# Optimization experiments

Hardware: AMD Instinct MI355X
Metric: run time of the kernel (lower is better)

The kernel has to match this reference:

```python
import jax, jax.numpy as jnp
import numpy as np
from jax import lax

K = 3
EPS = 1e-5


def get_graph_feature(x, k):
    # Faithful to the torch code, including flat .view() reshapes (no transpose)
    B, N = x.shape[0], x.shape[1]          # num_points = x.size(1)
    x = x.reshape(B, -1, N)                # (B, C, N) flat reshape
    C = x.shape[1]
    inner = -2.0 * jnp.einsum('bcn,bcm->bnm', x, x)           # (B, N, N)
    xx = jnp.sum(x * x, axis=1, keepdims=True)                # (B, 1, N)
    dist = -xx - inner - jnp.swapaxes(xx, 1, 2)               # neg sq distances
    idx = lax.top_k(dist, k)[1]                               # (B, N, k) nearest
    flat = x.reshape(B * N, C)                                # flat reshape (as torch .view)
    idx_full = (idx + (jnp.arange(B) * N)[:, None, None]).reshape(-1)
    feature = flat[idx_full].reshape(B, N, k, C)
    xc = x.reshape(B, N, 1, C)                                # flat reshape (as torch .view)
    feature = jnp.concatenate([feature - xc, jnp.broadcast_to(xc, (B, N, k, C))], axis=3)
    return feature.reshape(B, 2 * C, k, N)                    # flat reshape (as torch .view)


def bn(h, g, b, m, v, axis):
    shape = [1] * h.ndim
    shape[axis] = -1
    inv = g.reshape(shape) / jnp.sqrt(v.reshape(shape) + EPS)
    return (h - m.reshape(shape)) * inv + b.reshape(shape)


def setup_inputs() -> dict:
    key = jax.random.key(0)
    ks = jax.random.split(key, 24)
    B, N = 8, 4096

    def bn_params(i, c):
        return {
            f'bn{i}_g': jax.random.uniform(ks[4 * (ord(i) % 4)], (c,), jnp.float32) + 0.5,
            f'bn{i}_b': jax.random.normal(jax.random.fold_in(key, 10 + ord(i)), (c,), jnp.float32) * 0.1,
            f'bn{i}_m': jax.random.normal(jax.random.fold_in(key, 20 + ord(i)), (c,), jnp.float32) * 0.1,
            f'bn{i}_v': jax.random.uniform(jax.random.fold_in(key, 30 + ord(i)), (c,), jnp.float32) + 0.5,
        }

    inp = {
        'x': jax.random.normal(ks[0], (B, N, 3), jnp.float32),
        'w1': jax.random.normal(ks[1], (64, 6), jnp.float32) * (1.0 / np.sqrt(6.0)),
        'wA': jax.random.normal(ks[2], (256, 82), jnp.float32) * (1.0 / np.sqrt(82.0)),
        'bA': jax.random.normal(ks[3], (256,), jnp.float32) * 0.01,
        'wB': jax.random.normal(ks[4], (128, 256), jnp.float32) * (1.0 / np.sqrt(256.0)),
        'bB': jax.random.normal(ks[5], (128,), jnp.float32) * 0.01,
        'wC': jax.random.normal(ks[6], (3, 128), jnp.float32) * (1.0 / np.sqrt(128.0)),
        'bC': jax.random.normal(ks[7], (3,), jnp.float32) * 0.01,
    }
    inp.update(bn_params('1', 64))
    inp.update(bn_params('A', 256))
    inp.update(bn_params('B', 128))
    return inp


def reference(x, w1, wA, bA, wB, bB, wC, bC,
              bn1_g, bn1_b, bn1_m, bn1_v,
              bnA_g, bnA_b, bnA_m, bnA_v,
              bnB_g, bnB_b, bnB_m, bnB_v):
    f = get_graph_feature(x, K)                         # (B, 6, K, N)
    h = jnp.einsum('oc,bckn->bokn', w1, f)              # 1x1 conv, no bias
    h = jax.nn.leaky_relu(bn(h, bn1_g, bn1_b, bn1_m, bn1_v, 1), 0.2)
    x1 = jnp.max(h, axis=-1)                            # (B, 64, K)  (max over N!)
    x2 = jnp.max(get_graph_feature(x1, K), axis=-1)     # (B, 6, K)   (conv2 unused in source)
    x3 = jnp.max(get_graph_feature(x2, K), axis=-1)     # (B, 6, K)
    x4 = jnp.max(get_graph_feature(x3, K), axis=-1)     # (B, 6, K)
    xc = jnp.concatenate([x1, x2, x3, x4], axis=1)      # (B, 82, K)
    p = jnp.max(xc, axis=-1)                            # adaptive_max_pool1d -> (B, 82)
    h = jax.nn.leaky_relu(bn(p @ wA.T + bA, bnA_g, bnA_b, bnA_m, bnA_v, 1), 0.2)
    h = jax.nn.leaky_relu(bn(h @ wB.T + bB, bnB_g, bnB_b, bnB_m, bnB_v, 1), 0.2)
    return jax.nn.softmax(h @ wC.T + bC, axis=1)        # (B, 3)
```

## Files before the change

kernel.cpp:

```cpp
#include <hip/hip_runtime.h>
#include <math.h>

#define NPTS 4096
#define EPSV 1e-5f

__device__ __forceinline__ void top3_insert(float d, int m,
                                            float& d0, float& d1, float& d2,
                                            int& i0, int& i1, int& i2) {
  if (d > d2) {
    bool g1 = d > d1;
    bool g0 = d > d0;
    d2 = g1 ? d1 : d;                 i2 = g1 ? i1 : m;
    d1 = g0 ? d0 : (g1 ? d : d1);     i1 = g0 ? i0 : (g1 ? m : i1);
    d0 = g0 ? d : d0;                 i0 = g0 ? m : i0;
  }
}

__global__ __launch_bounds__(512) void k_knn1(const float* __restrict__ x,
                                              int* __restrict__ idx1) {
  __shared__ float4 pts[NPTS];
  __shared__ float cd[128][4][3];
  __shared__ int   ci[128][4][3];
  const int b   = blockIdx.x >> 5;
  const int blk = blockIdx.x & 31;
  const float* xb = x + b * (NPTS * 3);
  const int t = threadIdx.x;

  for (int m = t; m < NPTS; m += 512) {
    float a0 = xb[m], a1 = xb[NPTS + m], a2 = xb[2 * NPTS + m];
    float xx = a0 * a0; xx = fmaf(a1, a1, xx); xx = fmaf(a2, a2, xx);
    pts[m] = make_float4(a0, a1, a2, xx);
  }
  __syncthreads();

  const int p = t & 127;
  const int s = t >> 7;
  const int n = blk * 128 + p;
  const float4 pn = pts[n];
  const float c0 = -pn.w;
  float d0 = -INFINITY, d1 = -INFINITY, d2 = -INFINITY;
  int   i0 = 0x7fffffff, i1 = 0x7fffffff, i2 = 0x7fffffff;
  const int mstart = s * 1024;

  float4 qa[8];
#pragma unroll
  for (int j = 0; j < 8; ++j) qa[j] = pts[mstart + j];

  for (int mb = 0; mb < 1024; mb += 16) {
    float4 qb[8];
#pragma unroll
    for (int j = 0; j < 8; ++j) qb[j] = pts[mstart + mb + 8 + j];
#pragma unroll
    for (int j = 0; j < 8; ++j) {
      float4 q = qa[j];
      float dot = pn.x * q.x; dot = fmaf(pn.y, q.y, dot); dot = fmaf(pn.z, q.z, dot);
      float d = fmaf(2.0f, dot, c0) - q.w;
      top3_insert(d, mstart + mb + j, d0, d1, d2, i0, i1, i2);
    }
#pragma unroll
    for (int j = 0; j < 8; ++j) qa[j] = pts[mstart + ((mb + 16 + j) & 1023)];
#pragma unroll
    for (int j = 0; j < 8; ++j) {
      float4 q = qb[j];
      float dot = pn.x * q.x; dot = fmaf(pn.y, q.y, dot); dot = fmaf(pn.z, q.z, dot);
      float d = fmaf(2.0f, dot, c0) - q.w;
      top3_insert(d, mstart + mb + 8 + j, d0, d1, d2, i0, i1, i2);
    }
  }

  cd[p][s][0] = d0; cd[p][s][1] = d1; cd[p][s][2] = d2;
  ci[p][s][0] = i0; ci[p][s][1] = i1; ci[p][s][2] = i2;
  __syncthreads();

  if (t < 128) {
    int* op = idx1 + (b * NPTS + blk * 128 + t) * 3;
    float pd = INFINITY; int pi = -1;
    for (int r = 0; r < 3; ++r) {
      float bd = -INFINITY; int bi = 0x7fffffff;
      for (int sc = 0; sc < 4; ++sc) {
        for (int kk = 0; kk < 3; ++kk) {
          float dv = cd[t][sc][kk]; int iv = ci[t][sc][kk];
          bool allowed = (dv < pd) || (dv == pd && iv > pi);
          bool better  = (dv > bd) || (dv == bd && iv < bi);
          if (allowed && better) { bd = dv; bi = iv; }
        }
      }
      op[r] = bi;
      pd = bd; pi = bi;
    }
  }
}

__global__ __launch_bounds__(256) void k_convmax(const float* __restrict__ x,
                                                 const int* __restrict__ idx1,
                                                 const float* __restrict__ w1,
                                                 float* __restrict__ pmax) {
  __shared__ float4 Ft4[128][2];
  __shared__ float w1s[384];
  __shared__ float smax[4][64];
  const int b    = blockIdx.x / 96;
  const int rr   = blockIdx.x - b * 96;
  const int kk   = rr >> 5;
  const int tile = rr & 31;
  const int t = threadIdx.x;
  for (int i = t; i < 384; i += 256) w1s[i] = w1[i];
  const float* xb = x + b * 12288;
  const int*   ib = idx1 + b * 12288;

  const int tn = t & 127, ch = t >> 7;
  const int n = tile * 128 + tn;
  float* ftrow = (float*)&Ft4[tn][0];
#pragma unroll
  for (int j = 0; j < 3; ++j) {
    int c = ch * 3 + j;
    int ofs = c * 12288 + kk * 4096 + n;
    int np  = ofs / 18;
    int rem = ofs - np * 18;
    int kp  = rem / 6;
    int cp  = rem - kp * 6;
    float val;
    if (cp < 3) {
      int jj = ib[np * 3 + kp];
      val = xb[jj * 3 + cp] - xb[np * 3 + cp];
    } else {
      val = xb[np * 3 + cp - 3];
    }
    ftrow[c] = val;
  }
  __syncthreads();

  const int o = t & 63, sub = t >> 6;
  float w[6];
#pragma unroll
  for (int c = 0; c < 6; ++c) w[c] = w1s[o * 6 + c];
  const int base = sub * 32;
  float mx = -INFINITY;

  float4 ra[4][2];
#pragma unroll
  for (int r = 0; r < 4; ++r) { ra[r][0] = Ft4[base + r][0]; ra[r][1] = Ft4[base + r][1]; }

  for (int i = 0; i < 32; i += 8) {
    float4 rb[4][2];
#pragma unroll
    for (int r = 0; r < 4; ++r) {
      rb[r][0] = Ft4[base + i + 4 + r][0];
      rb[r][1] = Ft4[base + i + 4 + r][1];
    }
#pragma unroll
    for (int r = 0; r < 4; ++r) {
      float h = w[0] * ra[r][0].x;
      h = fmaf(w[1], ra[r][0].y, h);
      h = fmaf(w[2], ra[r][0].z, h);
      h = fmaf(w[3], ra[r][0].w, h);
      h = fmaf(w[4], ra[r][1].x, h);
      h = fmaf(w[5], ra[r][1].y, h);
      mx = fmaxf(mx, h);
    }
#pragma unroll
    for (int r = 0; r < 4; ++r) {
      int nr = base + ((i + 8 + r) & 31);
      ra[r][0] = Ft4[nr][0]; ra[r][1] = Ft4[nr][1];
    }
#pragma unroll
    for (int r = 0; r < 4; ++r) {
      float h = w[0] * rb[r][0].x;
      h = fmaf(w[1], rb[r][0].y, h);
      h = fmaf(w[2], rb[r][0].z, h);
      h = fmaf(w[3], rb[r][0].w, h);
      h = fmaf(w[4], rb[r][1].x, h);
      h = fmaf(w[5], rb[r][1].y, h);
      mx = fmaxf(mx, h);
    }
  }
  smax[sub][o] = mx;
  __syncthreads();
  if (t < 64) {
    float m01 = fmaxf(smax[0][t], smax[1][t]);
    float m23 = fmaxf(smax[2][t], smax[3][t]);
    pmax[((b * 3 + kk) * 64 + t) * 32 + tile] = fmaxf(m01, m23);
  }
}

__global__ __launch_bounds__(256) void k_tail(
    const float* __restrict__ pmax,
    const float* __restrict__ bn1g, const float* __restrict__ bn1b,
    const float* __restrict__ bn1m, const float* __restrict__ bn1v,
    const float* __restrict__ wA, const float* __restrict__ bA,
    const float* __restrict__ bnAg, const float* __restrict__ bnAb,
    const float* __restrict__ bnAm, const float* __restrict__ bnAv,
    const float* __restrict__ wB, const float* __restrict__ bB,
    const float* __restrict__ bnBg, const float* __restrict__ bnBb,
    const float* __restrict__ bnBm, const float* __restrict__ bnBv,
    const float* __restrict__ wC, const float* __restrict__ bC,
    float* __restrict__ out) {
  __shared__ float a1[192];
  __shared__ int   idx2[192];
  __shared__ float a2[18], a3[18], a4[18];
  __shared__ int   idxs[18];
  __shared__ float pv[82];
  __shared__ float hA[256];
  __shared__ float hB[128];
  __shared__ float lg[3];
  const int b = blockIdx.x;
  const int t = threadIdx.x;

  if (t < 192) {
    int o = t / 3, k = t - o * 3;
    const float4* p4 = (const float4*)(pmax + ((b * 3 + k) * 64 + o) * 32);
    float4 v[8];
#pragma unroll
    for (int j = 0; j < 8; ++j) v[j] = p4[j];
    float mx = -INFINITY;
#pragma unroll
    for (int j = 0; j < 8; ++j) {
      mx = fmaxf(mx, fmaxf(fmaxf(v[j].x, v[j].y), fmaxf(v[j].z, v[j].w)));
    }
    float inv = bn1g[o] / sqrtf(bn1v[o] + EPSV);
    float val = (mx - bn1m[o]) * inv + bn1b[o];
    a1[o * 3 + k] = val >= 0.f ? val : 0.2f * val;
  }
  __syncthreads();

  if (t < 64) {
    float px = a1[t], py = a1[64 + t], pz = a1[128 + t];
    float pp = px * px; pp = fmaf(py, py, pp); pp = fmaf(pz, pz, pp);
    float d0 = -INFINITY, d1 = -INFINITY, d2 = -INFINITY;
    int i0 = 0, i1 = 0, i2 = 0;
#pragma unroll 8
    for (int m = 0; m < 64; ++m) {
      float qx = a1[m], qy = a1[64 + m], qz = a1[128 + m];
      float qq = qx * qx; qq = fmaf(qy, qy, qq); qq = fmaf(qz, qz, qq);
      float dot = px * qx; dot = fmaf(py, qy, dot); dot = fmaf(pz, qz, dot);
      float d = 2.f * dot - pp - qq;
      top3_insert(d, m, d0, d1, d2, i0, i1, i2);
    }
    idx2[t * 3 + 0] = i0; idx2[t * 3 + 1] = i1; idx2[t * 3 + 2] = i2;
  }
  __syncthreads();

  if (t < 18) {
    int o = t / 3, kk = t - o * 3;
    float mx = -INFINITY;
#pragma unroll 8
    for (int nn = 0; nn < 64; ++nn) {
      int ofs = o * 192 + kk * 64 + nn;
      int np = ofs / 18; int rem = ofs - np * 18;
      int kp = rem / 6;  int cp  = rem - kp * 6;
      float val = (cp < 3) ? (a1[idx2[np * 3 + kp] * 3 + cp] - a1[np * 3 + cp])
                           : a1[np * 3 + cp - 3];
      mx = fmaxf(mx, val);
    }
    a2[t] = mx;
  }
  __syncthreads();

  for (int stage = 0; stage < 2; ++stage) {
    const float* src = (stage == 0) ? a2 : a3;
    float*       dst = (stage == 0) ? a3 : a4;
    if (t < 6) {
      float px = src[t], py = src[6 + t], pz = src[12 + t];
      float pp = px * px; pp = fmaf(py, py, pp); pp = fmaf(pz, pz, pp);
      float d0 = -INFINITY, d1 = -INFINITY, d2 = -INFINITY;
      int i0 = 0, i1 = 0, i2 = 0;
#pragma unroll
      for (int m = 0; m < 6; ++m) {
        float qx = src[m], qy = src[6 + m], qz = src[12 + m];
        float qq = qx * qx; qq = fmaf(qy, qy, qq); qq = fmaf(qz, qz, qq);
        float dot = px * qx; dot = fmaf(py, qy, dot); dot = fmaf(pz, qz, dot);
        float d = 2.f * dot - pp - qq;
        top3_insert(d, m, d0, d1, d2, i0, i1, i2);
      }
      idxs[t * 3 + 0] = i0; idxs[t * 3 + 1] = i1; idxs[t * 3 + 2] = i2;
    }
    __syncthreads();
    if (t < 18) {
      int o = t / 3, kk = t - o * 3;
      float mx = -INFINITY;
#pragma unroll
      for (int nn = 0; nn < 6; ++nn) {
        int ofs = o * 18 + kk * 6 + nn;
        int np = ofs / 18; int rem = ofs - np * 18;
        int kp = rem / 6;  int cp  = rem - kp * 6;
        float val = (cp < 3) ? (src[idxs[np * 3 + kp] * 3 + cp] - src[np * 3 + cp])
                             : src[np * 3 + cp - 3];
        mx = fmaxf(mx, val);
      }
      dst[t] = mx;
    }
    __syncthreads();
  }

  if (t < 82) {
    float mx;
    if (t < 64)      { int o = t;      mx = fmaxf(fmaxf(a1[o*3], a1[o*3+1]), a1[o*3+2]); }
    else if (t < 70) { int o = t - 64; mx = fmaxf(fmaxf(a2[o*3], a2[o*3+1]), a2[o*3+2]); }
    else if (t < 76) { int o = t - 70; mx = fmaxf(fmaxf(a3[o*3], a3[o*3+1]), a3[o*3+2]); }
    else             { int o = t - 76; mx = fmaxf(fmaxf(a4[o*3], a4[o*3+1]), a4[o*3+2]); }
    pv[t] = mx;
  }
  __syncthreads();

  {
    float acc = bA[t];
    const float* wr = wA + t * 82;
#pragma unroll 8
    for (int i = 0; i < 82; ++i) acc = fmaf(wr[i], pv[i], acc);
    float inv = bnAg[t] / sqrtf(bnAv[t] + EPSV);
    float v = (acc - bnAm[t]) * inv + bnAb[t];
    hA[t] = v >= 0.f ? v : 0.2f * v;
  }
  __syncthreads();

  if (t < 128) {
    float acc = bB[t];
    const float4* wr4 = (const float4*)(wB + t * 256);
#pragma unroll 8
    for (int i = 0; i < 64; ++i) {
      float4 wv = wr4[i];
      acc = fmaf(wv.x, hA[4 * i + 0], acc);
      acc = fmaf(wv.y, hA[4 * i + 1], acc);
      acc = fmaf(wv.z, hA[4 * i + 2], acc);
      acc = fmaf(wv.w, hA[4 * i + 3], acc);
    }
    float inv = bnBg[t] / sqrtf(bnBv[t] + EPSV);
    float v = (acc - bnBm[t]) * inv + bnBb[t];
    hB[t] = v >= 0.f ? v : 0.2f * v;
  }
  __syncthreads();

  if (t < 3) {
    float acc = bC[t];
    const float* wr = wC + t * 128;
#pragma unroll 8
    for (int i = 0; i < 128; ++i) acc = fmaf(wr[i], hB[i], acc);
    lg[t] = acc;
  }
  __syncthreads();
  if (t == 0) {
    float m = fmaxf(fmaxf(lg[0], lg[1]), lg[2]);
    float e0 = expf(lg[0] - m), e1 = expf(lg[1] - m), e2 = expf(lg[2] - m);
    float s = e0 + e1 + e2;
    out[b * 3 + 0] = e0 / s;
    out[b * 3 + 1] = e1 / s;
    out[b * 3 + 2] = e2 / s;
  }
}

extern "C" void kernel_launch(void* const* d_in, const int* in_sizes, int n_in,
                              void* d_out, int out_size, void* d_ws, size_t ws_size,
                              hipStream_t stream) {
  (void)in_sizes; (void)n_in; (void)out_size; (void)ws_size;
  const float* x    = (const float*)d_in[0];
  const float* w1   = (const float*)d_in[1];
  const float* wA   = (const float*)d_in[2];
  const float* bA   = (const float*)d_in[3];
  const float* wB   = (const float*)d_in[4];
  const float* bB   = (const float*)d_in[5];
  const float* wC   = (const float*)d_in[6];
  const float* bC   = (const float*)d_in[7];
  const float* bn1g = (const float*)d_in[8];
  const float* bn1b = (const float*)d_in[9];
  const float* bn1m = (const float*)d_in[10];
  const float* bn1v = (const float*)d_in[11];
  const float* bnAg = (const float*)d_in[12];
  const float* bnAb = (const float*)d_in[13];
  const float* bnAm = (const float*)d_in[14];
  const float* bnAv = (const float*)d_in[15];
  const float* bnBg = (const float*)d_in[16];
  const float* bnBb = (const float*)d_in[17];
  const float* bnBm = (const float*)d_in[18];
  const float* bnBv = (const float*)d_in[19];
  float* out = (float*)d_out;

  int*   idx1 = (int*)d_ws;
  float* pmax = (float*)((char*)d_ws + 8 * 4096 * 3 * 4);

  k_knn1<<<256, 512, 0, stream>>>(x, idx1);
  k_convmax<<<768, 256, 0, stream>>>(x, idx1, w1, pmax);
  k_tail<<<8, 256, 0, stream>>>(pmax,
                                bn1g, bn1b, bn1m, bn1v,
                                wA, bA, bnAg, bnAb, bnAm, bnAv,
                                wB, bB, bnBg, bnBb, bnBm, bnBv,
                                wC, bC, out);
}
```

Baseline: 187.1 us.

## Split kNN over more blocks and stage point cloud in LDS for conv gather

The kNN kernel now handles 64 query points per block with 8 candidate slices instead of 128 with 4. That doubles the grid to 512 blocks for better CU coverage, at the cost of reloading the point cloud into shared memory twice as often. The distance is refactored to pre-scaled coordinates in a nested fma chain. The conv/max kernel now copies the batch's whole point array into LDS with float4 loads, so the scattered neighbor gathers hit shared memory instead of global. That adds 48KB of LDS per block, which may limit occupancy.

```diff
diff --git a/kernel.cpp b/kernel.cpp
--- a/kernel.cpp
+++ b/kernel.cpp
@@ -4,25 +4,13 @@
 #define NPTS 4096
 #define EPSV 1e-5f
 
-__device__ __forceinline__ void top3_insert(float d, int m,
-                                            float& d0, float& d1, float& d2,
-                                            int& i0, int& i1, int& i2) {
-  if (d > d2) {
-    bool g1 = d > d1;
-    bool g0 = d > d0;
-    d2 = g1 ? d1 : d;                 i2 = g1 ? i1 : m;
-    d1 = g0 ? d0 : (g1 ? d : d1);     i1 = g0 ? i0 : (g1 ? m : i1);
-    d0 = g0 ? d : d0;                 i0 = g0 ? m : i0;
-  }
-}
-
-__global__ __launch_bounds__(512) void k_knn1(const float* __restrict__ x,
-                                              int* __restrict__ idx1) {
+__global__ __launch_bounds__(512, 4) void k_knn1(const float* __restrict__ x,
+                                                 int* __restrict__ idx1) {
   __shared__ float4 pts[NPTS];
-  __shared__ float cd[128][4][3];
-  __shared__ int   ci[128][4][3];
-  const int b   = blockIdx.x >> 5;
-  const int blk = blockIdx.x & 31;
+  __shared__ float cd[64][8][3];
+  __shared__ int   ci[64][8][3];
+  const int b   = blockIdx.x >> 6;
+  const int blk = blockIdx.x & 63;
   const float* xb = x + b * (NPTS * 3);
   const int t = threadIdx.x;
 
@@ -33,38 +21,49 @@
   }
   __syncthreads();
 
-  const int p = t & 127;
-  const int s = t >> 7;
-  const int n = blk * 128 + p;
+  const int p = t & 63;
+  const int s = t >> 6;
+  const int n = blk * 64 + p;
   const float4 pn = pts[n];
+  const float p2x = 2.0f * pn.x, p2y = 2.0f * pn.y, p2z = 2.0f * pn.z;
   const float c0 = -pn.w;
   float d0 = -INFINITY, d1 = -INFINITY, d2 = -INFINITY;
   int   i0 = 0x7fffffff, i1 = 0x7fffffff, i2 = 0x7fffffff;
-  const int mstart = s * 1024;
+  const int mstart = s * 512;
 
   float4 qa[8];
 #pragma unroll
   for (int j = 0; j < 8; ++j) qa[j] = pts[mstart + j];
 
-  for (int mb = 0; mb < 1024; mb += 16) {
+  for (int mb = 0; mb < 512; mb += 16) {
     float4 qb[8];
 #pragma unroll
     for (int j = 0; j < 8; ++j) qb[j] = pts[mstart + mb + 8 + j];
 #pragma unroll
     for (int j = 0; j < 8; ++j) {
       float4 q = qa[j];
-      float dot = pn.x * q.x; dot = fmaf(pn.y, q.y, dot); dot = fmaf(pn.z, q.z, dot);
-      float d = fmaf(2.0f, dot, c0) - q.w;
-      top3_insert(d, mstart + mb + j, d0, d1, d2, i0, i1, i2);
-    }
-#pragma unroll
-    for (int j = 0; j < 8; ++j) qa[j] = pts[mstart + ((mb + 16 + j) & 1023)];
+      float d = fmaf(p2x, q.x, fmaf(p2y, q.y, fmaf(p2z, q.z, c0))) - q.w;
+      if (d > d2) {
+        int m = mstart + mb + j;
+        bool g1 = d > d1, g0 = d > d0;
+        d2 = g1 ? d1 : d;               i2 = g1 ? i1 : m;
+        d1 = g0 ? d0 : (g1 ? d : d1);   i1 = g0 ? i0 : (g1 ? m : i1);
+        d0 = g0 ? d : d0;               i0 = g0 ? m : i0;
+      }
+    }
+#pragma unroll
+    for (int j = 0; j < 8; ++j) qa[j] = pts[mstart + ((mb + 16 + j) & 511)];
 #pragma unroll
     for (int j = 0; j < 8; ++j) {
       float4 q = qb[j];
-      float dot = pn.x * q.x; dot = fmaf(pn.y, q.y, dot); dot = fmaf(pn.z, q.z, dot);
-      float d = fmaf(2.0f, dot, c0) - q.w;
-      top3_insert(d, mstart + mb + 8 + j, d0, d1, d2, i0, i1, i2);
+      float d = fmaf(p2x, q.x, fmaf(p2y, q.y, fmaf(p2z, q.z, c0))) - q.w;
+      if (d > d2) {
+        int m = mstart + mb + 8 + j;
+        bool g1 = d > d1, g0 = d > d0;
+        d2 = g1 ? d1 : d;               i2 = g1 ? i1 : m;
+        d1 = g0 ? d0 : (g1 ? d : d1);   i1 = g0 ? i0 : (g1 ? m : i1);
+        d0 = g0 ? d : d0;               i0 = g0 ? m : i0;
+      }
     }
   }
 
@@ -72,12 +71,12 @@
   ci[p][s][0] = i0; ci[p][s][1] = i1; ci[p][s][2] = i2;
   __syncthreads();
 
-  if (t < 128) {
-    int* op = idx1 + (b * NPTS + blk * 128 + t) * 3;
+  if (t < 64) {
+    int* op = idx1 + (b * NPTS + blk * 64 + t) * 3;
     float pd = INFINITY; int pi = -1;
     for (int r = 0; r < 3; ++r) {
       float bd = -INFINITY; int bi = 0x7fffffff;
-      for (int sc = 0; sc < 4; ++sc) {
+      for (int sc = 0; sc < 8; ++sc) {
         for (int kk = 0; kk < 3; ++kk) {
           float dv = cd[t][sc][kk]; int iv = ci[t][sc][kk];
           bool allowed = (dv < pd) || (dv == pd && iv > pi);
@@ -91,21 +90,28 @@
   }
 }
 
-__global__ __launch_bounds__(256) void k_convmax(const float* __restrict__ x,
-                                                 const int* __restrict__ idx1,
-                                                 const float* __restrict__ w1,
-                                                 float* __restrict__ pmax) {
+__global__ __launch_bounds__(256, 2) void k_convmax(const float* __restrict__ x,
+                                                    const int* __restrict__ idx1,
+                                                    const float* __restrict__ w1,
+                                                    float* __restrict__ pmax) {
+  __shared__ float  xs[12288];
   __shared__ float4 Ft4[128][2];
-  __shared__ float w1s[384];
-  __shared__ float smax[4][64];
+  __shared__ float  w1s[384];
+  __shared__ float  smax[4][64];
   const int b    = blockIdx.x / 96;
   const int rr   = blockIdx.x - b * 96;
   const int kk   = rr >> 5;
   const int tile = rr & 31;
   const int t = threadIdx.x;
   for (int i = t; i < 384; i += 256) w1s[i] = w1[i];
-  const float* xb = x + b * 12288;
-  const int*   ib = idx1 + b * 12288;
+  {
+    const float4* xb4 = (const float4*)(x + b * 12288);
+    float4* xs4 = (float4*)xs;
+#pragma unroll
+    for (int i = 0; i < 12; ++i) xs4[t + 256 * i] = xb4[t + 256 * i];
+  }
+  const int* ib = idx1 + b * 12288;
+  __syncthreads();
 
   const int tn = t & 127, ch = t >> 7;
   const int n = tile * 128 + tn;
@@ -121,9 +127,9 @@
     float val;
     if (cp < 3) {
       int jj = ib[np * 3 + kp];
-      val = xb[jj * 3 + cp] - xb[np * 3 + cp];
+      val = xs[jj * 3 + cp] - xs[np * 3 + cp];
     } else {
-      val = xb[np * 3 + cp - 3];
+      val = xs[np * 3 + cp - 3];
     }
     ftrow[c] = val;
   }
@@ -179,6 +185,18 @@
     float m01 = fmaxf(smax[0][t], smax[1][t]);
     float m23 = fmaxf(smax[2][t], smax[3][t]);
     pmax[((b * 3 + kk) * 64 + t) * 32 + tile] = fmaxf(m01, m23);
+  }
+}
+
+__device__ __forceinline__ void top3_insert(float d, int m,
+                                            float& d0, float& d1, float& d2,
+                                            int& i0, int& i1, int& i2) {
+  if (d > d2) {
+    bool g1 = d > d1;
+    bool g0 = d > d0;
+    d2 = g1 ? d1 : d;                 i2 = g1 ? i1 : m;
+    d1 = g0 ? d0 : (g1 ? d : d1);     i1 = g0 ? i0 : (g1 ? m : i1);
+    d0 = g0 ? d : d0;                 i0 = g0 ? m : i0;
   }
 }
 
@@ -376,7 +394,7 @@
   int*   idx1 = (int*)d_ws;
   float* pmax = (float*)((char*)d_ws + 8 * 4096 * 3 * 4);
 
-  k_knn1<<<256, 512, 0, stream>>>(x, idx1);
+  k_knn1<<<512, 512, 0, stream>>>(x, idx1);
   k_convmax<<<768, 256, 0, stream>>>(x, idx1, w1, pmax);
   k_tail<<<8, 256, 0, stream>>>(pmax,
                                 bn1g, bn1b, bn1m, bn1v,
```

New measurement: 181.6 us. 1.03x faster.

## Rewrite kNN as group-max threshold filter with candidate recompute

Applied to the files above, without the earlier changes.

Replaces the per-thread running top-3 insertion over all 4096 points with a two-pass scheme. The first pass computes distances for 64 query points against 8 stored points per thread and reduces per-16-lane group maxima with DPP. A per-query third-largest group max then serves as a pruning threshold, and a second pass collects only points above it into small candidate lists, from which exact top-3 is recomputed. This removes the branchy insertion from the hot loop at the cost of recomputing distances, shared-memory atomics, and a cap of 24 candidates that could drop true neighbours on ties.

```diff
diff --git a/kernel.cpp b/kernel.cpp
--- a/kernel.cpp
+++ b/kernel.cpp
@@ -4,86 +4,147 @@
 #define NPTS 4096
 #define EPSV 1e-5f
 
-__device__ __forceinline__ void top3_insert(float d, int m,
-                                            float& d0, float& d1, float& d2,
-                                            int& i0, int& i1, int& i2) {
-  if (d > d2) {
-    bool g1 = d > d1;
-    bool g0 = d > d0;
-    d2 = g1 ? d1 : d;                 i2 = g1 ? i1 : m;
-    d1 = g0 ? d0 : (g1 ? d : d1);     i1 = g0 ? i0 : (g1 ? m : i1);
-    d0 = g0 ? d : d0;                 i0 = g0 ? m : i0;
-  }
-}
-
-__global__ __launch_bounds__(512) void k_knn1(const float* __restrict__ x,
-                                              int* __restrict__ idx1) {
-  __shared__ float4 pts[NPTS];
-  __shared__ float cd[128][4][3];
-  __shared__ int   ci[128][4][3];
-  const int b   = blockIdx.x >> 5;
-  const int blk = blockIdx.x & 31;
+template <int CTRL>
+__device__ __forceinline__ float dpp_max(float v) {
+#if __has_builtin(__builtin_amdgcn_update_dpp)
+  int o = __builtin_amdgcn_update_dpp(0, __float_as_int(v), CTRL, 0xF, 0xF, true);
+  return fmaxf(v, __int_as_float(o));
+#else
+  int lanemask = (CTRL == 0xB1) ? 1 : (CTRL == 0x4E) ? 2 : (CTRL == 0x141) ? 7 : 15;
+  return fmaxf(v, __shfl_xor(v, lanemask, 16));
+#endif
+}
+
+__global__ __launch_bounds__(512, 4) void k_knn1(const float* __restrict__ x,
+                                                 int* __restrict__ idx1) {
+  __shared__ float qxs[NPTS], qys[NPTS], qzs[NPTS];
+  __shared__ float4 ppre[68];
+  __shared__ float scmax[65][32];
+  __shared__ float theta[65];
+  __shared__ int   cnt[64];
+  __shared__ int   cands[64][24];
+  const int b     = blockIdx.x >> 6;
+  const int pr    = blockIdx.x & 63;
+  const int pbase = pr * 64;
   const float* xb = x + b * (NPTS * 3);
   const int t = threadIdx.x;
-
-  for (int m = t; m < NPTS; m += 512) {
-    float a0 = xb[m], a1 = xb[NPTS + m], a2 = xb[2 * NPTS + m];
-    float xx = a0 * a0; xx = fmaf(a1, a1, xx); xx = fmaf(a2, a2, xx);
-    pts[m] = make_float4(a0, a1, a2, xx);
-  }
-  __syncthreads();
-
-  const int p = t & 127;
-  const int s = t >> 7;
-  const int n = blk * 128 + p;
-  const float4 pn = pts[n];
-  const float c0 = -pn.w;
-  float d0 = -INFINITY, d1 = -INFINITY, d2 = -INFINITY;
-  int   i0 = 0x7fffffff, i1 = 0x7fffffff, i2 = 0x7fffffff;
-  const int mstart = s * 1024;
-
-  float4 qa[8];
-#pragma unroll
-  for (int j = 0; j < 8; ++j) qa[j] = pts[mstart + j];
-
-  for (int mb = 0; mb < 1024; mb += 16) {
-    float4 qb[8];
-#pragma unroll
-    for (int j = 0; j < 8; ++j) qb[j] = pts[mstart + mb + 8 + j];
-#pragma unroll
-    for (int j = 0; j < 8; ++j) {
-      float4 q = qa[j];
-      float dot = pn.x * q.x; dot = fmaf(pn.y, q.y, dot); dot = fmaf(pn.z, q.z, dot);
-      float d = fmaf(2.0f, dot, c0) - q.w;
-      top3_insert(d, mstart + mb + j, d0, d1, d2, i0, i1, i2);
-    }
-#pragma unroll
-    for (int j = 0; j < 8; ++j) qa[j] = pts[mstart + ((mb + 16 + j) & 1023)];
-#pragma unroll
-    for (int j = 0; j < 8; ++j) {
-      float4 q = qb[j];
-      float dot = pn.x * q.x; dot = fmaf(pn.y, q.y, dot); dot = fmaf(pn.z, q.z, dot);
-      float d = fmaf(2.0f, dot, c0) - q.w;
-      top3_insert(d, mstart + mb + 8 + j, d0, d1, d2, i0, i1, i2);
-    }
-  }
-
-  cd[p][s][0] = d0; cd[p][s][1] = d1; cd[p][s][2] = d2;
-  ci[p][s][0] = i0; ci[p][s][1] = i1; ci[p][s][2] = i2;
-  __syncthreads();
-
-  if (t < 128) {
-    int* op = idx1 + (b * NPTS + blk * 128 + t) * 3;
+  const int g = t >> 4;
+
+  float qx[8], qy[8], qz[8], qw[8];
+  {
+    const float4* X = (const float4*)(xb + 8 * t);
+    const float4* Y = (const float4*)(xb + NPTS + 8 * t);
+    const float4* Z = (const float4*)(xb + 2 * NPTS + 8 * t);
+    float4 x0 = X[0], x1 = X[1];
+    float4 y0 = Y[0], y1 = Y[1];
+    float4 z0 = Z[0], z1 = Z[1];
+    qx[0] = x0.x; qx[1] = x0.y; qx[2] = x0.z; qx[3] = x0.w;
+    qx[4] = x1.x; qx[5] = x1.y; qx[6] = x1.z; qx[7] = x1.w;
+    qy[0] = y0.x; qy[1] = y0.y; qy[2] = y0.z; qy[3] = y0.w;
+    qy[4] = y1.x; qy[5] = y1.y; qy[6] = y1.z; qy[7] = y1.w;
+    qz[0] = z0.x; qz[1] = z0.y; qz[2] = z0.z; qz[3] = z0.w;
+    qz[4] = z1.x; qz[5] = z1.y; qz[6] = z1.z; qz[7] = z1.w;
+    *(float4*)&qxs[8 * t] = x0; *(float4*)&qxs[8 * t + 4] = x1;
+    *(float4*)&qys[8 * t] = y0; *(float4*)&qys[8 * t + 4] = y1;
+    *(float4*)&qzs[8 * t] = z0; *(float4*)&qzs[8 * t + 4] = z1;
+  }
+#pragma unroll
+  for (int j = 0; j < 8; ++j)
+    qw[j] = -fmaf(qz[j], qz[j], fmaf(qy[j], qy[j], qx[j] * qx[j]));
+  if (t < 64) cnt[t] = 0;
+  __syncthreads();
+  if (t < 64) {
+    float px = qxs[pbase + t], py = qys[pbase + t], pz = qzs[pbase + t];
+    ppre[t] = make_float4(2.f * px, 2.f * py, 2.f * pz, 0.f);
+  } else if (t < 68) {
+    ppre[t] = make_float4(0.f, 0.f, 0.f, 0.f);
+  }
+  __syncthreads();
+
+  auto proc = [&](float4 P, int p) {
+    float k0 = fmaf(P.x, qx[0], fmaf(P.y, qy[0], fmaf(P.z, qz[0], qw[0])));
+    float k1 = fmaf(P.x, qx[1], fmaf(P.y, qy[1], fmaf(P.z, qz[1], qw[1])));
+    float k2 = fmaf(P.x, qx[2], fmaf(P.y, qy[2], fmaf(P.z, qz[2], qw[2])));
+    float k3 = fmaf(P.x, qx[3], fmaf(P.y, qy[3], fmaf(P.z, qz[3], qw[3])));
+    float k4 = fmaf(P.x, qx[4], fmaf(P.y, qy[4], fmaf(P.z, qz[4], qw[4])));
+    float k5 = fmaf(P.x, qx[5], fmaf(P.y, qy[5], fmaf(P.z, qz[5], qw[5])));
+    float k6 = fmaf(P.x, qx[6], fmaf(P.y, qy[6], fmaf(P.z, qz[6], qw[6])));
+    float k7 = fmaf(P.x, qx[7], fmaf(P.y, qy[7], fmaf(P.z, qz[7], qw[7])));
+    float v = fmaxf(fmaxf(fmaxf(k0, k1), fmaxf(k2, k3)),
+                    fmaxf(fmaxf(k4, k5), fmaxf(k6, k7)));
+    v = dpp_max<0xB1>(v);
+    v = dpp_max<0x4E>(v);
+    v = dpp_max<0x141>(v);
+    v = dpp_max<0x140>(v);
+    if ((t & 15) == 0) scmax[p][g] = v;
+  };
+  {
+    float4 pp0 = ppre[0], pp1 = ppre[1], pp2 = ppre[2], pp3 = ppre[3];
+    for (int p0 = 0; p0 < 64; p0 += 4) {
+      float4 n0 = ppre[p0 + 4], n1 = ppre[p0 + 5];
+      float4 n2 = ppre[p0 + 6], n3 = ppre[p0 + 7];
+      proc(pp0, p0 + 0); proc(pp1, p0 + 1);
+      proc(pp2, p0 + 2); proc(pp3, p0 + 3);
+      pp0 = n0; pp1 = n1; pp2 = n2; pp3 = n3;
+    }
+  }
+  __syncthreads();
+
+  if (t < 64) {
+    const float4* row = (const float4*)scmax[t];
+    float d0 = -INFINITY, d1 = -INFINITY, d2 = -INFINITY;
+#pragma unroll
+    for (int q4 = 0; q4 < 8; ++q4) {
+      float4 vv = row[q4];
+      float va[4] = {vv.x, vv.y, vv.z, vv.w};
+#pragma unroll
+      for (int u = 0; u < 4; ++u) {
+        float v = va[u];
+        float nd2 = fmaxf(d2, fminf(d1, v));
+        float nd1 = fmaxf(d1, fminf(d0, v));
+        d0 = fmaxf(d0, v); d1 = nd1; d2 = nd2;
+      }
+    }
+    theta[t] = d2;
+  }
+  __syncthreads();
+
+  {
+    float gm = scmax[0][g], th = theta[0];
+    for (int p = 0; p < 64; ++p) {
+      float ngm = scmax[p + 1][g];
+      float nth = theta[p + 1];
+      if (gm >= th) {
+        float4 P = ppre[p];
+#pragma unroll
+        for (int j = 0; j < 8; ++j) {
+          float kj = fmaf(P.x, qx[j], fmaf(P.y, qy[j], fmaf(P.z, qz[j], qw[j])));
+          if (kj >= th) {
+            int c = atomicAdd(&cnt[p], 1);
+            if (c < 24) cands[p][c] = 8 * t + j;
+          }
+        }
+      }
+      gm = ngm; th = nth;
+    }
+  }
+  __syncthreads();
+
+  if (t < 64) {
+    int c = cnt[t]; if (c > 24) c = 24;
+    const float4 P = ppre[t];
+    int* op = idx1 + (b * NPTS + pbase + t) * 3;
     float pd = INFINITY; int pi = -1;
     for (int r = 0; r < 3; ++r) {
       float bd = -INFINITY; int bi = 0x7fffffff;
-      for (int sc = 0; sc < 4; ++sc) {
-        for (int kk = 0; kk < 3; ++kk) {
-          float dv = cd[t][sc][kk]; int iv = ci[t][sc][kk];
-          bool allowed = (dv < pd) || (dv == pd && iv > pi);
-          bool better  = (dv > bd) || (dv == bd && iv < bi);
-          if (allowed && better) { bd = dv; bi = iv; }
-        }
+      for (int cc = 0; cc < c; ++cc) {
+        int m = cands[t][cc];
+        float mxv = qxs[m], myv = qys[m], mzv = qzs[m];
+        float mw = -fmaf(mzv, mzv, fmaf(myv, myv, mxv * mxv));
+        float kv = fmaf(P.x, mxv, fmaf(P.y, myv, fmaf(P.z, mzv, mw)));
+        bool allowed = (kv < pd) || (kv == pd && m > pi);
+        bool better  = (kv > bd) || (kv == bd && m < bi);
+        if (allowed && better) { bd = kv; bi = m; }
       }
       op[r] = bi;
       pd = bd; pi = bi;
@@ -96,8 +157,8 @@
                                                  const float* __restrict__ w1,
                                                  float* __restrict__ pmax) {
   __shared__ float4 Ft4[128][2];
-  __shared__ float w1s[384];
-  __shared__ float smax[4][64];
+  __shared__ float  w1s[384];
+  __shared__ float  smax[4][64];
   const int b    = blockIdx.x / 96;
   const int rr   = blockIdx.x - b * 96;
   const int kk   = rr >> 5;
@@ -179,6 +240,18 @@
     float m01 = fmaxf(smax[0][t], smax[1][t]);
     float m23 = fmaxf(smax[2][t], smax[3][t]);
     pmax[((b * 3 + kk) * 64 + t) * 32 + tile] = fmaxf(m01, m23);
+  }
+}
+
+__device__ __forceinline__ void top3_insert(float d, int m,
+                                            float& d0, float& d1, float& d2,
+                                            int& i0, int& i1, int& i2) {
+  if (d > d2) {
+    bool g1 = d > d1;
+    bool g0 = d > d0;
+    d2 = g1 ? d1 : d;                 i2 = g1 ? i1 : m;
+    d1 = g0 ? d0 : (g1 ? d : d1);     i1 = g0 ? i0 : (g1 ? m : i1);
+    d0 = g0 ? d : d0;                 i0 = g0 ? m : i0;
   }
 }
 
@@ -376,7 +449,7 @@
   int*   idx1 = (int*)d_ws;
   float* pmax = (float*)((char*)d_ws + 8 * 4096 * 3 * 4);
 
-  k_knn1<<<256, 512, 0, stream>>>(x, idx1);
+  k_knn1<<<512, 512, 0, stream>>>(x, idx1);
   k_convmax<<<768, 256, 0, stream>>>(x, idx1, w1, pmax);
   k_tail<<<8, 256, 0, stream>>>(pmax,
                                 bn1g, bn1b, bn1m, bn1v,
```

Measured after the change: 177.9 us. -4.9%, faster.
